# Kernel optimization log

Measured on AMD Instinct MI355X. Metric: run time of the kernel, lower is better.

## Reference

```python
import jax, jax.numpy as jnp
import numpy as np

B, S, H, NH = 8, 1042, 768, 12
HD = H // NH            # 64
P = 1024                # patch tokens (32x32 grid); RoPE applied to last P tokens
MLP = 2048              # int(768 * 8/3)
EPS = 1e-6


def _rope_tables():
    # mirrors precompute_rope_freqs_2d(HD, P): inside, dim = HD//2 = 32
    dim = HD // 2
    t = int(P ** 0.5)  # 32
    freqs = 1.0 / (10000.0 ** (np.arange(0, dim, 2, dtype=np.float32) / dim))  # (16,)
    pos = np.arange(t, dtype=np.float32)
    fh = pos[:, None] * freqs[None, :]                       # (t,16)
    f = np.concatenate([np.tile(fh[:, None, :], (1, t, 1)),
                        np.tile(fh[None, :, :], (t, 1, 1))], axis=-1)  # (t,t,32)
    f = f.reshape(P, dim)                                    # (1024,32)
    return jnp.asarray(np.cos(f)), jnp.asarray(np.sin(f))


def setup_inputs() -> dict:
    key = jax.random.key(0)
    ks = jax.random.split(key, 20)
    r = lambda k, sh, sc: (jax.random.normal(k, sh, jnp.float32) * sc)
    cos, sin = _rope_tables()
    return {
        "x": jax.random.normal(ks[0], (B, S, H), jnp.float32),
        "rope_cos": cos, "rope_sin": sin,
        "Wq": r(ks[1], (H, H), 0.02), "Wk": r(ks[2], (H, H), 0.02),
        "Wv": r(ks[3], (H, H), 0.02), "Wo": r(ks[4], (H, H), 0.02),
        "q_norm_w": jnp.ones((HD,), jnp.float32),
        "k_norm_w": jnp.ones((HD,), jnp.float32),
        "gate_W": r(ks[5], (H, NH), 0.02),
        "gate_b": jnp.full((NH,), 4.0, jnp.float32),
        "norm1_w": jnp.ones((H,), jnp.float32),
        "norm2_w": jnp.ones((H,), jnp.float32),
        "W_gate": r(ks[6], (H, MLP), 0.02),
        "W_up": r(ks[7], (H, MLP), 0.02),
        "W_down": r(ks[8], (MLP, H), 0.02),
        "attn_scale": r(ks[9], (H,), 0.1),   # zero-init in module; randn for nontrivial grads
        "mlp_scale": r(ks[10], (H,), 0.1),
    }


def _rmsnorm(x, w):
    return x * jax.lax.rsqrt(jnp.mean(x * x, axis=-1, keepdims=True) + EPS) * w


def _apply_rope(x, cos, sin):
    # x: (B,S,NH,HD); rotate only the last P (patch) tokens, consecutive-pair complex rotation
    xp = x[:, -P:].reshape(B, P, NH, HD // 2, 2)
    x0, x1 = xp[..., 0], xp[..., 1]
    c = cos[None, :, None, :]
    s = sin[None, :, None, :]
    rot = jnp.stack([x0 * c - x1 * s, x0 * s + x1 * c], axis=-1).reshape(B, P, NH, HD)
    return jnp.concatenate([x[:, :-P], rot], axis=1)


def reference(x, rope_cos, rope_sin, Wq, Wk, Wv, Wo, q_norm_w, k_norm_w,
              gate_W, gate_b, norm1_w, norm2_w, W_gate, W_up, W_down,
              attn_scale, mlp_scale):
    # --- attention branch (QwenGatedRoPEAttention) ---
    h = _rmsnorm(x, norm1_w)
    q = (h @ Wq).reshape(B, S, NH, HD)
    k = (h @ Wk).reshape(B, S, NH, HD)
    v = (h @ Wv).reshape(B, S, NH, HD)
    q = _rmsnorm(q, q_norm_w)
    k = _rmsnorm(k, k_norm_w)
    q = _apply_rope(q, rope_cos, rope_sin)
    k = _apply_rope(k, rope_cos, rope_sin)
    q = q / jnp.sqrt(jnp.asarray(HD, jnp.float32))
    scores = jnp.einsum('bqhd,bkhd->bhqk', q, k)          # (B,NH,S,S)
    probs = jax.nn.softmax(scores.astype(jnp.float32), axis=-1)
    attn = jnp.einsum('bhqk,bkhd->bqhd', probs, v)        # (B,S,NH,HD)
    gate = jax.nn.sigmoid((h @ gate_W)[..., None] + gate_b[None, None, :, None])
    attn = (attn * gate).reshape(B, S, H)
    x = x + (attn @ Wo) * attn_scale
    # --- SwiGLU MLP branch ---
    h2 = _rmsnorm(x, norm2_w)
    mlp = (jax.nn.silu(h2 @ W_gate) * (h2 @ W_up)) @ W_down
    x = x + mlp * mlp_scale
    return x
```

## Files before the change

kernel.cpp:

```cpp
#include <hip/hip_runtime.h>
#include <hip/hip_bf16.h>
#include <stdint.h>

#define B_   8
#define S_   1042
#define H_   768
#define NH_  12
#define HD_  64
#define MLP_ 2048
#define T_   (B_*S_)
#define MP_  8448
#define SP_  1088
#define EPS_ 1e-6f

typedef __attribute__((ext_vector_type(8))) short bf16x8v;
typedef __attribute__((ext_vector_type(4))) float f32x4;
typedef __hip_bfloat16 bf16;

typedef __attribute__((address_space(1))) const void gas_void;
typedef __attribute__((address_space(3))) void las_void;

__device__ inline void gload_lds16(const void* g, void* l) {
  __builtin_amdgcn_global_load_lds((gas_void*)g, (las_void*)l, 16, 0, 0);
}

#define BARRIER asm volatile("s_barrier" ::: "memory")
#define VMCNT4  asm volatile("s_waitcnt vmcnt(4)" ::: "memory")
#define VMCNT0  asm volatile("s_waitcnt vmcnt(0)" ::: "memory")

__global__ __launch_bounds__(256) void wcvt_t(const float* __restrict__ W, bf16* __restrict__ o,
                                              int K, int N) {
  __shared__ float tile[32][33];
  int kt = blockIdx.x, nt = blockIdx.y;
  int t = threadIdx.x;
  int r = t >> 5, c = t & 31;
#pragma unroll
  for (int i = 0; i < 4; i++)
    tile[i * 8 + r][c] = W[(long)(kt * 32 + i * 8 + r) * N + nt * 32 + c];
  __syncthreads();
#pragma unroll
  for (int i = 0; i < 4; i++)
    o[(long)(nt * 32 + i * 8 + r) * K + kt * 32 + c] = __float2bfloat16(tile[c][i * 8 + r]);
}

__global__ __launch_bounds__(256) void wcvt_gu(const float* __restrict__ Wg,
                                               const float* __restrict__ Wu,
                                               bf16* __restrict__ o) {
  __shared__ float tile[32][33];
  int kt = blockIdx.x, nt = blockIdx.y;
  int t = threadIdx.x;
  int r = t >> 5, c = t & 31;
  const float* src = (c < 16) ? Wg : Wu;
  int col = nt * 16 + (c & 15);
#pragma unroll
  for (int i = 0; i < 4; i++)
    tile[i * 8 + r][c] = src[(long)(kt * 32 + i * 8 + r) * MLP_ + col];
  __syncthreads();
#pragma unroll
  for (int i = 0; i < 4; i++)
    o[(long)(nt * 32 + i * 8 + r) * 768 + kt * 32 + c] = __float2bfloat16(tile[c][i * 8 + r]);
}

template <int GATE>
__global__ __launch_bounds__(256) void rmsnorm_k(const float* __restrict__ x,
                                                 const float* __restrict__ w,
                                                 bf16* __restrict__ o,
                                                 const float* __restrict__ gW,
                                                 const float* __restrict__ gb,
                                                 float* __restrict__ gate, int Mreal) {
  int row = blockIdx.x;
  bf16* orow = o + (long)row * H_;
  int t = threadIdx.x;
  if (row >= Mreal) {
    for (int i = t; i < H_; i += 256) orow[i] = __float2bfloat16(0.f);
    return;
  }
  const float* xr = x + (long)row * H_;
  float v0 = xr[t], v1 = xr[t + 256], v2 = xr[t + 512];
  float s = v0 * v0 + v1 * v1 + v2 * v2;
  for (int off = 32; off; off >>= 1) s += __shfl_down(s, off);
  __shared__ float red[4];
  __shared__ float gred[4][12];
  if ((t & 63) == 0) red[t >> 6] = s;
  __syncthreads();
  float tot = red[0] + red[1] + red[2] + red[3];
  float inv = rsqrtf(tot * (1.f / H_) + EPS_);
  float h0 = v0 * inv * w[t], h1 = v1 * inv * w[t + 256], h2 = v2 * inv * w[t + 512];
  orow[t]       = __float2bfloat16(h0);
  orow[t + 256] = __float2bfloat16(h1);
  orow[t + 512] = __float2bfloat16(h2);
  if (GATE) {
    const float* g0 = gW + (long)t * 12;
    const float* g1 = gW + (long)(t + 256) * 12;
    const float* g2 = gW + (long)(t + 512) * 12;
    float g[12];
#pragma unroll
    for (int n = 0; n < 12; n++) g[n] = h0 * g0[n] + h1 * g1[n] + h2 * g2[n];
#pragma unroll
    for (int n = 0; n < 12; n++) {
      float v = g[n];
      v += __shfl_xor(v, 1); v += __shfl_xor(v, 2); v += __shfl_xor(v, 4);
      v += __shfl_xor(v, 8); v += __shfl_xor(v, 16); v += __shfl_xor(v, 32);
      if ((t & 63) == 0) gred[t >> 6][n] = v;
    }
    __syncthreads();
    if (t < 12) {
      float s4 = gred[0][t] + gred[1][t] + gred[2][t] + gred[3][t];
      gate[(long)row * 12 + t] = 1.f / (1.f + __expf(-(s4 + gb[t])));
    }
  }
}

template <int EPI, int KT, int LD>
__global__ __launch_bounds__(512) void gemm256(
    const bf16* __restrict__ A, const bf16* __restrict__ Bt, void* __restrict__ Out,
    const float* __restrict__ resid, const float* __restrict__ scale,
    int N, int nbn, int Mreal) {
  __shared__ __align__(16) bf16 lds[2][4][128 * 64];
  int tid = threadIdx.x;
  int lane = tid & 63, wid = tid >> 6;
  int wr = wid >> 2, wc = wid & 3;
  int lr = lane & 15, lg = lane >> 4;

  int nwg = gridDim.x;
  int bid = blockIdx.x;
  int q = nwg >> 3, r8 = nwg & 7;
  int xcd = bid & 7, idx = bid >> 3;
  int wg = (xcd < r8 ? xcd * (q + 1) : r8 * (q + 1) + (xcd - r8) * q) + idx;
  int bm = wg / nbn, bn = wg - bm * nbn;

  const bf16 *aP0[2], *aP1[2], *bP0[2], *bP1[2];
  {
    int off0 = lr * 64 + ((lg ^ (lr & 7)) * 8);
    int off1 = lr * 64 + (((4 + lg) ^ (lr & 7)) * 8);
#pragma unroll
    for (int b = 0; b < 2; b++) {
      aP0[b] = &lds[b][wr][off0];
      aP1[b] = &lds[b][wr][off1];
      bP0[b] = &lds[b][2 + (wc >> 1)][(wc & 1) * 4096 + off0];
      bP1[b] = &lds[b][2 + (wc >> 1)][(wc & 1) * 4096 + off1];
    }
  }
  int chunk_row = tid >> 3;
  int cc = (tid & 7) ^ (chunk_row & 7);
  const bf16 *aB[2][2], *bB[2][2];
#pragma unroll
  for (int h = 0; h < 2; h++)
#pragma unroll
    for (int sub = 0; sub < 2; sub++) {
      aB[h][sub] = A + ((long)bm * 256 + h * 128 + sub * 64 + chunk_row) * LD + cc * 8;
      bB[h][sub] = Bt + ((long)bn * 256 + h * 128 + sub * 64 + chunk_row) * LD + cc * 8;
    }

#define STA(buf, half, kt)                                                      \
  {                                                                             \
    gload_lds16(aB[half][0] + (kt) * 64, &lds[buf][half][tid * 8]);             \
    gload_lds16(aB[half][1] + (kt) * 64, &lds[buf][half][4096 + tid * 8]);      \
  }
#define STB(buf, half, kt)                                                      \
  {                                                                             \
    gload_lds16(bB[half][0] + (kt) * 64, &lds[buf][2 + (half)][tid * 8]);       \
    gload_lds16(bB[half][1] + (kt) * 64, &lds[buf][2 + (half)][4096 + tid * 8]);\
  }

  f32x4 z; z[0] = z[1] = z[2] = z[3] = 0.f;
  f32x4 acc[8][4];
#pragma unroll
  for (int mi = 0; mi < 8; mi++)
#pragma unroll
    for (int ni = 0; ni < 4; ni++) acc[mi][ni] = z;

  bf16x8v bf[4][2];
  bf16x8v af[4];

  STA(0, 0, 0); STA(0, 1, 0); STB(0, 0, 0); STB(0, 1, 0);
  STB(1, 0, 1); STB(1, 1, 1);
  VMCNT4;
  BARRIER;

#define PHASE(p, bb, STG, VM)                                                   \
  {                                                                             \
    if ((p) == 0) {                                                             \
      _Pragma("unroll") for (int ni = 0; ni < 4; ni++) {                        \
        bf[ni][0] = *(const bf16x8v*)(bP0[bb] + ni * 1024);                     \
        bf[ni][1] = *(const bf16x8v*)(bP1[bb] + ni * 1024);                     \
      }                                                                         \
    }                                                                           \
    af[0] = *(const bf16x8v*)(aP0[bb] + (2 * (p)) * 1024);                      \
    af[1] = *(const bf16x8v*)(aP1[bb] + (2 * (p)) * 1024);                      \
    af[2] = *(const bf16x8v*)(aP0[bb] + (2 * (p) + 1) * 1024);                  \
    af[3] = *(const bf16x8v*)(aP1[bb] + (2 * (p) + 1) * 1024);                  \
    STG;                                                                        \
    BARRIER;                                                                    \
    __builtin_amdgcn_s_setprio(1);                                              \
    _Pragma("unroll") for (int dm = 0; dm < 2; dm++)                            \
      _Pragma("unroll") for (int ni = 0; ni < 4; ni++) {                        \
        acc[2 * (p) + dm][ni] = __builtin_amdgcn_mfma_f32_16x16x32_bf16(        \
            af[dm * 2 + 0], bf[ni][0], acc[2 * (p) + dm][ni], 0, 0, 0);         \
        acc[2 * (p) + dm][ni] = __builtin_amdgcn_mfma_f32_16x16x32_bf16(        \
            af[dm * 2 + 1], bf[ni][1], acc[2 * (p) + dm][ni], 0, 0, 0);         \
      }                                                                         \
    __builtin_amdgcn_s_setprio(0);                                              \
    if (VM) VMCNT4;                                                             \
  }

#define ITERBODY(i)                                                             \
  {                                                                             \
    int u = 2 * (i) + 1;                                                        \
    int t2 = (2 * (i) + 2 < KT) ? 2 * (i) + 2 : KT - 1;                         \
    int t3 = (2 * (i) + 3 < KT) ? 2 * (i) + 3 : KT - 1;                         \
    PHASE(0, 0, STA(1, 0, u), 0);                                               \
    PHASE(1, 0, STA(1, 1, u), 0);                                               \
    PHASE(2, 0, STB(0, 0, t2), 0);                                              \
    PHASE(3, 0, STB(0, 1, t2), 1);                                              \
    PHASE(0, 1, STA(0, 0, t2), 0);                                              \
    PHASE(1, 1, STA(0, 1, t2), 0);                                              \
    PHASE(2, 1, STB(1, 0, t3), 0);                                              \
    PHASE(3, 1, STB(1, 1, t3), 1);                                              \
  }

  if (KT <= 12) {
#pragma unroll
    for (int i = 0; i < KT / 2; i++) ITERBODY(i);
  } else {
#pragma unroll 2
    for (int i = 0; i < KT / 2; i++) ITERBODY(i);
  }
  VMCNT0;
#undef ITERBODY
#undef PHASE
#undef STA
#undef STB

  long rowbase = (long)bm * 256 + wr * 128;
  int colbase = bn * 256 + wc * 64;
  if (EPI == 0) {
    bf16* O = (bf16*)Out;
#pragma unroll
    for (int mi = 0; mi < 8; mi++)
#pragma unroll
      for (int ni = 0; ni < 4; ni++)
#pragma unroll
        for (int r = 0; r < 4; r++)
          O[(rowbase + mi * 16 + lg * 4 + r) * N + colbase + ni * 16 + lr] =
              __float2bfloat16(acc[mi][ni][r]);
  } else if (EPI == 1) {
    float* O = (float*)Out;
#pragma unroll
    for (int ni = 0; ni < 4; ni++) {
      float sc = scale[colbase + ni * 16 + lr];
#pragma unroll
      for (int mi = 0; mi < 8; mi++)
#pragma unroll
        for (int r = 0; r < 4; r++) {
          long row = rowbase + mi * 16 + lg * 4 + r;
          long col = colbase + ni * 16 + lr;
          if (row < Mreal)
            O[row * N + col] = resid[row * N + col] + acc[mi][ni][r] * sc;
        }
    }
  } else {
    bf16* O = (bf16*)Out;
    int oc0 = colbase >> 1;
#pragma unroll
    for (int mi = 0; mi < 8; mi++)
#pragma unroll
      for (int p = 0; p < 2; p++)
#pragma unroll
        for (int r = 0; r < 4; r++) {
          float g = acc[mi][2 * p][r], u = acc[mi][2 * p + 1][r];
          float v = g / (1.f + __expf(-g)) * u;
          O[(rowbase + mi * 16 + lg * 4 + r) * 2048 + oc0 + p * 16 + lr] =
              __float2bfloat16(v);
        }
  }
}

__global__ __launch_bounds__(256) void vtran(const bf16* __restrict__ qkv, bf16* __restrict__ vtf) {
  __shared__ bf16 tile[32][66];
  int st = blockIdx.x, bh = blockIdx.y;
  int bb = bh / NH_, h = bh - bb * NH_;
  int s0 = st * 32;
  int t = threadIdx.x;
  int si = t >> 6, d = t & 63;
#pragma unroll
  for (int i = 0; i < 8; i++) {
    int s = s0 + i * 4 + si;
    bf16 v = __float2bfloat16(0.f);
    if (s < S_) v = qkv[(long)(bb * S_ + s) * 2304 + 1536 + h * 64 + d];
    tile[i * 4 + si][d] = v;
  }
  __syncthreads();
  int dd = t >> 5, sj = t & 31;
#pragma unroll
  for (int i = 0; i < 8; i++) {
    int d2 = i * 8 + dd;
    vtf[((long)bh * 64 + d2) * SP_ + s0 + sj] = tile[sj][d2];
  }
}

__global__ __launch_bounds__(768) void qkv_post(
    const bf16* __restrict__ qkv, const float* __restrict__ qw, const float* __restrict__ kw,
    const float* __restrict__ cosT, const float* __restrict__ sinT,
    bf16* __restrict__ qf, bf16* __restrict__ kf) {
  int tok = blockIdx.x;
  int bb = tok / S_, s = tok - bb * S_;
  int h = threadIdx.x >> 6, d = threadIdx.x & 63;
  const bf16* base = qkv + (long)tok * 2304 + h * 64 + d;
  float q = __bfloat162float(base[0]);
  float k = __bfloat162float(base[768]);
  float qs = q * q, ks = k * k;
  for (int off = 32; off; off >>= 1) {
    qs += __shfl_xor(qs, off);
    ks += __shfl_xor(ks, off);
  }
  q *= rsqrtf(qs * (1.f / 64.f) + EPS_) * qw[d];
  k *= rsqrtf(ks * (1.f / 64.f) + EPS_) * kw[d];
  if (s >= S_ - 1024) {
    int pos = s - (S_ - 1024);
    int i = d >> 1;
    float c = cosT[pos * 32 + i], sn = sinT[pos * 32 + i];
    float qp = __shfl_xor(q, 1), kp = __shfl_xor(k, 1);
    if (d & 1) { q = qp * sn + q * c; k = kp * sn + k * c; }
    else       { q = q * c - qp * sn; k = k * c - kp * sn; }
  }
  q *= 0.125f * 1.44269504088896f;
  long o1 = ((long)(bb * NH_ + h) * SP_ + s) * 64 + d;
  qf[o1] = __float2bfloat16(q);
  kf[o1] = __float2bfloat16(k);
}

#define SWZ(row, cc) (((row) << 6) + ((((cc) ^ ((row) & 7))) << 3))

__global__ __launch_bounds__(256) void attn_k(
    const bf16* __restrict__ qf, const bf16* __restrict__ kf, const bf16* __restrict__ vtf,
    const float* __restrict__ gate, bf16* __restrict__ attn_g) {
  __shared__ __align__(16) bf16 Ks[2][64 * 64];
  __shared__ __align__(16) bf16 Vs[2][64 * 64];
  int bid = blockIdx.x;
  int w = (bid & 7) * 204 + (bid >> 3);
  int bh = w / 17, qb = w - bh * 17;
  int bb = bh / NH_, h = bh - bb * NH_;
  int tid = threadIdx.x;
  int lane = tid & 63, wv = tid >> 6;
  int lr = lane & 15, lg = lane >> 4;
  const bf16* qbase = qf + (long)bh * SP_ * 64;
  const bf16* kbase = kf + (long)bh * SP_ * 64;
  const bf16* vbase = vtf + (long)bh * 64 * SP_;

  int q_l = qb * 64 + wv * 16 + lr;
  bf16x8v qB0 = *(const bf16x8v*)(qbase + (long)q_l * 64 + lg * 8);
  bf16x8v qB1 = *(const bf16x8v*)(qbase + (long)q_l * 64 + 32 + lg * 8);

  f32x4 z; z[0] = z[1] = z[2] = z[3] = 0.f;
  f32x4 acc[4] = {z, z, z, z};
  float tsacc = 0.f;

  auto stage = [&](int buf, int kidx) {
#pragma unroll
    for (int inst = 0; inst < 2; inst++) {
      int c = inst * 256 + tid;
      int row = c >> 3, slot = c & 7;
      int cc = slot ^ (row & 7);
      gload_lds16(kbase + (long)(kidx + row) * 64 + cc * 8, &Ks[buf][c * 8]);
    }
#pragma unroll
    for (int inst = 0; inst < 2; inst++) {
      int c = inst * 256 + tid;
      int row = c >> 3, slot = c & 7;
      int cc = slot ^ (row & 7);
      gload_lds16(vbase + (long)row * SP_ + kidx + cc * 8, &Vs[buf][c * 8]);
    }
  };

  stage(0, 0);
  VMCNT0;
  __syncthreads();
  int cur = 0;

  for (int kt = 0; kt < SP_ / 64; kt++) {
    int kidx = kt * 64;
    if (kt < SP_ / 64 - 1) stage(cur ^ 1, kidx + 64);

    f32x4 p[4];
    __builtin_amdgcn_s_setprio(1);
#pragma unroll
    for (int mt = 0; mt < 4; mt++) {
      int row = mt * 16 + lr;
      bf16x8v k0 = *(const bf16x8v*)&Ks[cur][SWZ(row, lg)];
      bf16x8v k1 = *(const bf16x8v*)&Ks[cur][SWZ(row, lg + 4)];
      f32x4 t = z;
      t = __builtin_amdgcn_mfma_f32_16x16x32_bf16(k0, qB0, t, 0, 0, 0);
      t = __builtin_amdgcn_mfma_f32_16x16x32_bf16(k1, qB1, t, 0, 0, 0);
      p[mt] = t;
    }
    __builtin_amdgcn_s_setprio(0);

    if (kidx + 64 > S_) {
#pragma unroll
      for (int mt = 0; mt < 4; mt++)
#pragma unroll
        for (int r = 0; r < 4; r++)
          if (kidx + mt * 16 + lg * 4 + r >= S_) p[mt][r] = -1e30f;
    }

#pragma unroll
    for (int mt = 0; mt < 4; mt++)
#pragma unroll
      for (int r = 0; r < 4; r++) {
        float e = exp2f(p[mt][r]);
        p[mt][r] = e;
        tsacc += e;
      }

    uint32_t w0[4], w1[4];
#pragma unroll
    for (int mt = 0; mt < 4; mt++) {
      asm("v_cvt_pk_bf16_f32 %0, %1, %2" : "=v"(w0[mt]) : "v"(p[mt][0]), "v"(p[mt][1]));
      asm("v_cvt_pk_bf16_f32 %0, %1, %2" : "=v"(w1[mt]) : "v"(p[mt][2]), "v"(p[mt][3]));
    }
    bf16x8v aP[2];
#pragma unroll
    for (int t2 = 0; t2 < 2; t2++) {
      union { uint32_t u[4]; bf16x8v v; } cvt;
#pragma unroll
      for (int wd = 0; wd < 4; wd++) {
        uint32_t a = (wd & 1) ? w1[2 * t2] : w0[2 * t2];
        uint32_t b = (wd & 1) ? w1[2 * t2 + 1] : w0[2 * t2 + 1];
        uint32_t val = (lg & 2) ? b : a;
        int src = ((lg & 1) * 2 + (wd >> 1)) * 16 + lr;
        cvt.u[wd] = (uint32_t)__shfl((int)val, src);
      }
      aP[t2] = cvt.v;
    }
    __builtin_amdgcn_s_setprio(1);
#pragma unroll
    for (int t2 = 0; t2 < 2; t2++)
#pragma unroll
      for (int dt = 0; dt < 4; dt++) {
        int row = dt * 16 + lr;
        bf16x8v vB = *(const bf16x8v*)&Vs[cur][SWZ(row, t2 * 4 + lg)];
        acc[dt] = __builtin_amdgcn_mfma_f32_16x16x32_bf16(aP[t2], vB, acc[dt], 0, 0, 0);
      }
    __builtin_amdgcn_s_setprio(0);

    VMCNT0;
    __syncthreads();
    cur ^= 1;
  }

  tsacc += __shfl_xor(tsacc, 16);
  tsacc += __shfl_xor(tsacc, 32);
  float norm = 0.f;
  if (q_l < S_) norm = gate[((long)bb * S_ + q_l) * 12 + h] / tsacc;
  float nr[4];
#pragma unroll
  for (int r = 0; r < 4; r++) nr[r] = __shfl(norm, lg * 4 + r);
#pragma unroll
  for (int dt = 0; dt < 4; dt++)
#pragma unroll
    for (int r = 0; r < 4; r++) {
      int qr = qb * 64 + wv * 16 + lg * 4 + r;
      if (qr < S_)
        attn_g[((long)bb * S_ + qr) * H_ + h * 64 + dt * 16 + lr] =
            __float2bfloat16(acc[dt][r] * nr[r]);
    }
}

extern "C" void kernel_launch(void* const* d_in, const int* in_sizes, int n_in,
                              void* d_out, int out_size, void* d_ws, size_t ws_size,
                              hipStream_t stream) {
  const float* x    = (const float*)d_in[0];
  const float* cosT = (const float*)d_in[1];
  const float* sinT = (const float*)d_in[2];
  const float* Wq   = (const float*)d_in[3];
  const float* Wk   = (const float*)d_in[4];
  const float* Wv   = (const float*)d_in[5];
  const float* Wo   = (const float*)d_in[6];
  const float* qnw  = (const float*)d_in[7];
  const float* knw  = (const float*)d_in[8];
  const float* gW   = (const float*)d_in[9];
  const float* gb   = (const float*)d_in[10];
  const float* n1w  = (const float*)d_in[11];
  const float* n2w  = (const float*)d_in[12];
  const float* Wg   = (const float*)d_in[13];
  const float* Wu   = (const float*)d_in[14];
  const float* Wd   = (const float*)d_in[15];
  const float* ascale = (const float*)d_in[16];
  const float* mscale = (const float*)d_in[17];

  char* ws = (char*)d_ws;
  size_t off = 0;
  auto alloc = [&](size_t bytes) {
    char* p = ws + off;
    off += (bytes + 255) & ~(size_t)255;
    return p;
  };
  bf16* h_pad  = (bf16*)alloc((size_t)MP_ * H_ * 2);
  bf16* wqkv_t = (bf16*)alloc((size_t)2304 * 768 * 2);
  bf16* wo_t   = (bf16*)alloc((size_t)768 * 768 * 2);
  bf16* wgu_t  = (bf16*)alloc((size_t)4096 * 768 * 2);
  bf16* wdn_t  = (bf16*)alloc((size_t)768 * 2048 * 2);
  bf16* qkv    = (bf16*)alloc((size_t)MP_ * 2304 * 2);
  bf16* qfb    = (bf16*)alloc((size_t)96 * SP_ * 64 * 2);
  bf16* kfb    = (bf16*)alloc((size_t)96 * SP_ * 64 * 2);
  bf16* vtfb   = (bf16*)alloc((size_t)96 * SP_ * 64 * 2);
  float* gateb = (float*)alloc((size_t)T_ * 12 * 4);
  bf16* attn_g = (bf16*)alloc((size_t)MP_ * H_ * 2);
  float* x2    = (float*)alloc((size_t)T_ * H_ * 4);
  bf16* mlpin  = qkv;

  auto wc = [&](const float* W, bf16* o, int K, int N) {
    wcvt_t<<<dim3(K / 32, N / 32), 256, 0, stream>>>(W, o, K, N);
  };
  wc(Wq, wqkv_t, 768, 768);
  wc(Wk, wqkv_t + 768 * 768, 768, 768);
  wc(Wv, wqkv_t + 2 * 768 * 768, 768, 768);
  wc(Wo, wo_t, 768, 768);
  wc(Wd, wdn_t, 2048, 768);
  wcvt_gu<<<dim3(24, 128), 256, 0, stream>>>(Wg, Wu, wgu_t);

  rmsnorm_k<1><<<MP_, 256, 0, stream>>>(x, n1w, h_pad, gW, gb, gateb, T_);

  gemm256<0, 12, 768><<<9 * 33, 512, 0, stream>>>(h_pad, wqkv_t, qkv, nullptr, nullptr,
                                                  2304, 9, MP_);

  qkv_post<<<T_, 768, 0, stream>>>(qkv, qnw, knw, cosT, sinT, qfb, kfb);
  vtran<<<dim3(33, 96), 256, 0, stream>>>(qkv, vtfb);

  attn_k<<<1632, 256, 0, stream>>>(qfb, kfb, vtfb, gateb, attn_g);

  gemm256<1, 12, 768><<<3 * 33, 512, 0, stream>>>(attn_g, wo_t, x2, x, ascale,
                                                  768, 3, T_);

  rmsnorm_k<0><<<MP_, 256, 0, stream>>>(x2, n2w, h_pad, nullptr, nullptr, nullptr, T_);

  gemm256<2, 12, 768><<<16 * 33, 512, 0, stream>>>(h_pad, wgu_t, mlpin, nullptr, nullptr,
                                                   4096, 16, MP_);

  gemm256<1, 32, 2048><<<3 * 33, 512, 0, stream>>>(mlpin, wdn_t, (float*)d_out, x2, mscale,
                                                   768, 3, T_);
}
```

Measured before the change: 408.6 us.

## Halve GEMM K-tile depth and split-K the down-projection with a separate reduce

The GEMM kernel's K-step shrinks from 64 to 32, which halves LDS use per stage and adjusts the swizzle, load macros and wait counts to match. The down-projection GEMM, which launched only 99 workgroups, is split four ways along K (396 workgroups) to fill more compute units. Its bf16 partial sums go to reused scratch buffers, and a new reduce kernel adds them together and applies the residual and scale. This trades extra memory traffic, an extra launch and bf16 rounding of the partials for better occupancy and a lower LDS footprint.

```diff
diff --git a/kernel.cpp b/kernel.cpp
--- a/kernel.cpp
+++ b/kernel.cpp
@@ -12,6 +12,7 @@
 #define MP_  8448
 #define SP_  1088
 #define EPS_ 1e-6f
+#define PSLICE ((long)96 * SP_ * 64)
 
 typedef __attribute__((ext_vector_type(8))) short bf16x8v;
 typedef __attribute__((ext_vector_type(4))) float f32x4;
@@ -25,7 +26,7 @@
 }
 
 #define BARRIER asm volatile("s_barrier" ::: "memory")
-#define VMCNT4  asm volatile("s_waitcnt vmcnt(4)" ::: "memory")
+#define VMCNT2  asm volatile("s_waitcnt vmcnt(2)" ::: "memory")
 #define VMCNT0  asm volatile("s_waitcnt vmcnt(0)" ::: "memory")
 
 __global__ __launch_bounds__(256) void wcvt_t(const float* __restrict__ W, bf16* __restrict__ o,
@@ -111,12 +112,12 @@
   }
 }
 
-template <int EPI, int KT, int LD>
+template <int EPI, int KT, int LD, int NKS>
 __global__ __launch_bounds__(512) void gemm256(
     const bf16* __restrict__ A, const bf16* __restrict__ Bt, void* __restrict__ Out,
     const float* __restrict__ resid, const float* __restrict__ scale,
-    int N, int nbn, int Mreal) {
-  __shared__ __align__(16) bf16 lds[2][4][128 * 64];
+    int N, int nbn, int Mreal, bf16* __restrict__ alt3) {
+  __shared__ __align__(16) bf16 lds[2][4][128 * 32];
   int tid = threadIdx.x;
   int lane = tid & 63, wid = tid >> 6;
   int wr = wid >> 2, wc = wid & 3;
@@ -127,41 +128,37 @@
   int q = nwg >> 3, r8 = nwg & 7;
   int xcd = bid & 7, idx = bid >> 3;
   int wg = (xcd < r8 ? xcd * (q + 1) : r8 * (q + 1) + (xcd - r8) * q) + idx;
+
+  int ks = 0;
+  if (NKS > 1) {
+    int bps = nwg / NKS;
+    ks = wg / bps;
+    wg = wg - ks * bps;
+    A += (long)ks * KT * 32;
+    Bt += (long)ks * KT * 32;
+  }
   int bm = wg / nbn, bn = wg - bm * nbn;
 
-  const bf16 *aP0[2], *aP1[2], *bP0[2], *bP1[2];
+  const bf16 *aP[2], *bP[2];
   {
-    int off0 = lr * 64 + ((lg ^ (lr & 7)) * 8);
-    int off1 = lr * 64 + (((4 + lg) ^ (lr & 7)) * 8);
+    int off = lr * 32 + ((lg ^ ((lr >> 1) & 3)) * 8);
 #pragma unroll
     for (int b = 0; b < 2; b++) {
-      aP0[b] = &lds[b][wr][off0];
-      aP1[b] = &lds[b][wr][off1];
-      bP0[b] = &lds[b][2 + (wc >> 1)][(wc & 1) * 4096 + off0];
-      bP1[b] = &lds[b][2 + (wc >> 1)][(wc & 1) * 4096 + off1];
-    }
-  }
-  int chunk_row = tid >> 3;
-  int cc = (tid & 7) ^ (chunk_row & 7);
-  const bf16 *aB[2][2], *bB[2][2];
-#pragma unroll
-  for (int h = 0; h < 2; h++)
-#pragma unroll
-    for (int sub = 0; sub < 2; sub++) {
-      aB[h][sub] = A + ((long)bm * 256 + h * 128 + sub * 64 + chunk_row) * LD + cc * 8;
-      bB[h][sub] = Bt + ((long)bn * 256 + h * 128 + sub * 64 + chunk_row) * LD + cc * 8;
-    }
-
-#define STA(buf, half, kt)                                                      \
-  {                                                                             \
-    gload_lds16(aB[half][0] + (kt) * 64, &lds[buf][half][tid * 8]);             \
-    gload_lds16(aB[half][1] + (kt) * 64, &lds[buf][half][4096 + tid * 8]);      \
-  }
-#define STB(buf, half, kt)                                                      \
-  {                                                                             \
-    gload_lds16(bB[half][0] + (kt) * 64, &lds[buf][2 + (half)][tid * 8]);       \
-    gload_lds16(bB[half][1] + (kt) * 64, &lds[buf][2 + (half)][4096 + tid * 8]);\
-  }
+      aP[b] = &lds[b][wr][off];
+      bP[b] = &lds[b][2 + (wc >> 1)][(wc & 1) * 2048 + off];
+    }
+  }
+  int srow = tid >> 2;
+  int cc = (tid & 3) ^ ((srow >> 1) & 3);
+  const bf16 *aB[2], *bB[2];
+#pragma unroll
+  for (int h = 0; h < 2; h++) {
+    aB[h] = A + ((long)bm * 256 + h * 128 + srow) * LD + cc * 8;
+    bB[h] = Bt + ((long)bn * 256 + h * 128 + srow) * LD + cc * 8;
+  }
+
+#define STA(buf, half, kt) gload_lds16(aB[half] + (kt) * 32, &lds[buf][half][tid * 8]);
+#define STB(buf, half, kt) gload_lds16(bB[half] + (kt) * 32, &lds[buf][2 + (half)][tid * 8]);
 
   f32x4 z; z[0] = z[1] = z[2] = z[3] = 0.f;
   f32x4 acc[8][4];
@@ -170,38 +167,31 @@
 #pragma unroll
     for (int ni = 0; ni < 4; ni++) acc[mi][ni] = z;
 
-  bf16x8v bf[4][2];
-  bf16x8v af[4];
+  bf16x8v bf[4];
+  bf16x8v af[2];
 
   STA(0, 0, 0); STA(0, 1, 0); STB(0, 0, 0); STB(0, 1, 0);
   STB(1, 0, 1); STB(1, 1, 1);
-  VMCNT4;
+  VMCNT2;
   BARRIER;
 
 #define PHASE(p, bb, STG, VM)                                                   \
   {                                                                             \
     if ((p) == 0) {                                                             \
-      _Pragma("unroll") for (int ni = 0; ni < 4; ni++) {                        \
-        bf[ni][0] = *(const bf16x8v*)(bP0[bb] + ni * 1024);                     \
-        bf[ni][1] = *(const bf16x8v*)(bP1[bb] + ni * 1024);                     \
-      }                                                                         \
+      _Pragma("unroll") for (int ni = 0; ni < 4; ni++)                          \
+        bf[ni] = *(const bf16x8v*)(bP[bb] + ni * 512);                          \
     }                                                                           \
-    af[0] = *(const bf16x8v*)(aP0[bb] + (2 * (p)) * 1024);                      \
-    af[1] = *(const bf16x8v*)(aP1[bb] + (2 * (p)) * 1024);                      \
-    af[2] = *(const bf16x8v*)(aP0[bb] + (2 * (p) + 1) * 1024);                  \
-    af[3] = *(const bf16x8v*)(aP1[bb] + (2 * (p) + 1) * 1024);                  \
+    af[0] = *(const bf16x8v*)(aP[bb] + (2 * (p)) * 512);                        \
+    af[1] = *(const bf16x8v*)(aP[bb] + (2 * (p) + 1) * 512);                    \
     STG;                                                                        \
     BARRIER;                                                                    \
     __builtin_amdgcn_s_setprio(1);                                              \
     _Pragma("unroll") for (int dm = 0; dm < 2; dm++)                            \
-      _Pragma("unroll") for (int ni = 0; ni < 4; ni++) {                        \
+      _Pragma("unroll") for (int ni = 0; ni < 4; ni++)                          \
         acc[2 * (p) + dm][ni] = __builtin_amdgcn_mfma_f32_16x16x32_bf16(        \
-            af[dm * 2 + 0], bf[ni][0], acc[2 * (p) + dm][ni], 0, 0, 0);         \
-        acc[2 * (p) + dm][ni] = __builtin_amdgcn_mfma_f32_16x16x32_bf16(        \
-            af[dm * 2 + 1], bf[ni][1], acc[2 * (p) + dm][ni], 0, 0, 0);         \
-      }                                                                         \
+            af[dm], bf[ni], acc[2 * (p) + dm][ni], 0, 0, 0);                    \
     __builtin_amdgcn_s_setprio(0);                                              \
-    if (VM) VMCNT4;                                                             \
+    if (VM) VMCNT2;                                                             \
   }
 
 #define ITERBODY(i)                                                             \
@@ -235,7 +225,9 @@
   long rowbase = (long)bm * 256 + wr * 128;
   int colbase = bn * 256 + wc * 64;
   if (EPI == 0) {
-    bf16* O = (bf16*)Out;
+    bf16* O;
+    if (NKS > 1) O = (ks < 3) ? (bf16*)Out + (long)ks * PSLICE : alt3;
+    else O = (bf16*)Out;
 #pragma unroll
     for (int mi = 0; mi < 8; mi++)
 #pragma unroll
@@ -274,6 +266,39 @@
               __float2bfloat16(v);
         }
   }
+}
+
+__global__ __launch_bounds__(256) void mlp2_reduce(
+    const bf16* __restrict__ p012, const bf16* __restrict__ p3,
+    const float* __restrict__ x2, const float* __restrict__ mscale,
+    float* __restrict__ out) {
+  long i = (long)blockIdx.x * 256 + threadIdx.x;
+  long row = i / 96;
+  int c8 = (int)(i - row * 96) * 8;
+  long off = row * 768 + c8;
+  float a[8];
+#pragma unroll
+  for (int j = 0; j < 8; j++) a[j] = 0.f;
+#pragma unroll
+  for (int s = 0; s < 3; s++) {
+    bf16x8v v = *(const bf16x8v*)(p012 + s * PSLICE + off);
+#pragma unroll
+    for (int j = 0; j < 8; j++) {
+      short sv = v[j];
+      a[j] += __bfloat162float(*reinterpret_cast<bf16*>(&sv));
+    }
+  }
+  {
+    bf16x8v v = *(const bf16x8v*)(p3 + off);
+#pragma unroll
+    for (int j = 0; j < 8; j++) {
+      short sv = v[j];
+      a[j] += __bfloat162float(*reinterpret_cast<bf16*>(&sv));
+    }
+  }
+#pragma unroll
+  for (int j = 0; j < 8; j++)
+    out[off + j] = x2[off + j] + a[j] * mscale[c8 + j];
 }
 
 __global__ __launch_bounds__(256) void vtran(const bf16* __restrict__ qkv, bf16* __restrict__ vtf) {
@@ -502,9 +527,9 @@
   bf16* wgu_t  = (bf16*)alloc((size_t)4096 * 768 * 2);
   bf16* wdn_t  = (bf16*)alloc((size_t)768 * 2048 * 2);
   bf16* qkv    = (bf16*)alloc((size_t)MP_ * 2304 * 2);
-  bf16* qfb    = (bf16*)alloc((size_t)96 * SP_ * 64 * 2);
-  bf16* kfb    = (bf16*)alloc((size_t)96 * SP_ * 64 * 2);
-  bf16* vtfb   = (bf16*)alloc((size_t)96 * SP_ * 64 * 2);
+  bf16* qfb    = (bf16*)alloc((size_t)PSLICE * 2);
+  bf16* kfb    = (bf16*)alloc((size_t)PSLICE * 2);
+  bf16* vtfb   = (bf16*)alloc((size_t)PSLICE * 2);
   float* gateb = (float*)alloc((size_t)T_ * 12 * 4);
   bf16* attn_g = (bf16*)alloc((size_t)MP_ * H_ * 2);
   float* x2    = (float*)alloc((size_t)T_ * H_ * 4);
@@ -522,22 +547,23 @@
 
   rmsnorm_k<1><<<MP_, 256, 0, stream>>>(x, n1w, h_pad, gW, gb, gateb, T_);
 
-  gemm256<0, 12, 768><<<9 * 33, 512, 0, stream>>>(h_pad, wqkv_t, qkv, nullptr, nullptr,
-                                                  2304, 9, MP_);
+  gemm256<0, 24, 768, 1><<<9 * 33, 512, 0, stream>>>(h_pad, wqkv_t, qkv, nullptr, nullptr,
+                                                     2304, 9, MP_, nullptr);
 
   qkv_post<<<T_, 768, 0, stream>>>(qkv, qnw, knw, cosT, sinT, qfb, kfb);
   vtran<<<dim3(33, 96), 256, 0, stream>>>(qkv, vtfb);
 
   attn_k<<<1632, 256, 0, stream>>>(qfb, kfb, vtfb, gateb, attn_g);
 
-  gemm256<1, 12, 768><<<3 * 33, 512, 0, stream>>>(attn_g, wo_t, x2, x, ascale,
-                                                  768, 3, T_);
+  gemm256<1, 24, 768, 1><<<3 * 33, 512, 0, stream>>>(attn_g, wo_t, x2, x, ascale,
+                                                     768, 3, T_, nullptr);
 
   rmsnorm_k<0><<<MP_, 256, 0, stream>>>(x2, n2w, h_pad, nullptr, nullptr, nullptr, T_);
 
-  gemm256<2, 12, 768><<<16 * 33, 512, 0, stream>>>(h_pad, wgu_t, mlpin, nullptr, nullptr,
-                                                   4096, 16, MP_);
-
-  gemm256<1, 32, 2048><<<3 * 33, 512, 0, stream>>>(mlpin, wdn_t, (float*)d_out, x2, mscale,
-                                                   768, 3, T_);
-}
+  gemm256<2, 24, 768, 1><<<16 * 33, 512, 0, stream>>>(h_pad, wgu_t, mlpin, nullptr, nullptr,
+                                                      4096, 16, MP_, nullptr);
+
+  gemm256<0, 16, 2048, 4><<<4 * 3 * 33, 512, 0, stream>>>(mlpin, wdn_t, qfb, nullptr, nullptr,
+                                                          768, 3, MP_, attn_g);
+  mlp2_reduce<<<(T_ * 96) / 256, 256, 0, stream>>>(qfb, attn_g, x2, mscale, (float*)d_out);
+}
```

Result: faster. 392.6 us (-3.9%).
